# Performance work log

Hardware: AMD Instinct MI355X
Metric: run time of the kernel (lower is better)

Reference implementation:

```python
import jax, jax.numpy as jnp
import numpy as np
import math

BS, L, NNF, NEF = 8, 107, 17, 9
NH, EH, H3, NL, K = 128, 32, 32, 10, 3
PC, TL, TH, FF, NCLS = 32, 3, 8, 256, 3
D = NH + PC
HD = D // TH
RPG = 150
N = BS * L
E = BS * (2 * (L - 1) + RPG)
EPS = 1e-5


def _ln(z, g, b):
    m = z.mean(-1, keepdims=True)
    v = ((z - m) ** 2).mean(-1, keepdims=True)
    return (z - m) / jnp.sqrt(v + EPS) * g + b


def _gelu(z):
    return jax.nn.gelu(z, approximate=False)


def _forward(x, edge_attr, cheb_w, cheb_b, ee_w, ee_b, mlp_w1, mlp_b1, mlp_w2, mlp_b2,
             root_w, conv_b, ln_g, ln_b, attn_in_w, attn_in_b, attn_out_w, attn_out_b,
             ff_w1, ff_b1, ff_w2, ff_b2, tln1_g, tln1_b, tln2_g, tln2_b, lin_w, lin_b,
             seq_edge_index, edge_index):
    n = x.shape[0]
    # --- ChebConv (K=3, sym norm, lambda_max=2 -> L_hat = -D^-1/2 A D^-1/2) on seq edges ---
    ss, sd = seq_edge_index[0], seq_edge_index[1]
    deg = jax.ops.segment_sum(jnp.ones_like(ss, dtype=x.dtype), ss, num_segments=n)
    dinv = jnp.where(deg > 0, jax.lax.rsqrt(jnp.maximum(deg, 1e-12)), 0.0)
    w = -(dinv[ss] * dinv[sd])
    lap = lambda h: jax.ops.segment_sum(w[:, None] * h[ss], sd, num_segments=n)
    tx1 = lap(x)
    tx2 = 2.0 * lap(tx1) - x
    h = x @ cheb_w[0] + tx1 @ cheb_w[1] + tx2 @ cheb_w[2] + cheb_b

    # --- edge encoder ---
    ea = edge_attr @ ee_w + ee_b
    src, dst = edge_index[0], edge_index[1]

    # --- NNConv: per-edge weight W_e = MLP(ea) in R^{NHxNH}; gather-matmul-scatter ---
    def nnconv(h, l):
        we = ((ea @ mlp_w1[l] + mlp_b1[l]) @ mlp_w2[l] + mlp_b2[l]).reshape(-1, NH, NH)
        msg = jnp.einsum('ei,eio->eo', h[src], we)
        return jax.ops.segment_sum(msg, dst, num_segments=n) + h @ root_w[l] + conv_b[l]

    h = nnconv(h, 0)  # layers[0].conv applied directly (no residual)
    for l in range(1, NL):  # DeepGCNLayer res+: x + conv(gelu(LN(x)))
        h = h + nnconv(_gelu(_ln(h, ln_g[l], ln_b[l])), l)
    h = _gelu(_ln(h, ln_g[0], ln_b[0]))  # reuses layer 0's norm/act

    # --- sinusoidal position encoding (dim=PC), concat ---
    p = jnp.arange(L, dtype=x.dtype)[:, None]
    div = jnp.exp(jnp.arange(0, PC, 2, dtype=x.dtype) * (-math.log(10000.0) / PC))
    pos = jnp.zeros((L, PC), dtype=x.dtype)
    pos = pos.at[:, 0::2].set(jnp.sin(p * div)).at[:, 1::2].set(jnp.cos(p * div))

    t = jnp.concatenate([h.reshape(BS, L, NH), jnp.broadcast_to(pos, (BS, L, PC))], -1)

    # --- post-norm TransformerEncoder (relu FFN), vectorized over graphs ---
    scale = 1.0 / math.sqrt(HD)
    for l in range(TL):
        qkv = t @ attn_in_w[l] + attn_in_b[l]
        q, k, v = jnp.split(qkv, 3, axis=-1)
        q = q.reshape(BS, L, TH, HD)
        k = k.reshape(BS, L, TH, HD)
        v = v.reshape(BS, L, TH, HD)
        a = jax.nn.softmax(jnp.einsum('bqhd,bkhd->bhqk', q, k) * scale, axis=-1)
        o = jnp.einsum('bhqk,bkhd->bqhd', a, v).reshape(BS, L, D) @ attn_out_w[l] + attn_out_b[l]
        t = _ln(t + o, tln1_g[l], tln1_b[l])
        f = jax.nn.relu(t @ ff_w1[l] + ff_b1[l]) @ ff_w2[l] + ff_b2[l]
        t = _ln(t + f, tln2_g[l], tln2_b[l])

    return t.reshape(n, D) @ lin_w + lin_b


def setup_inputs():
    rng = np.random.default_rng(0)
    ks = iter(jax.random.split(jax.random.key(0), 40))
    # bidirectional sequence edges per graph + random pair edges
    base = np.arange(L - 1)
    s = np.concatenate([base, base + 1])
    d = np.concatenate([base + 1, base])
    off = (np.arange(BS) * L)[:, None]
    seq_src = (s[None] + off).ravel()
    seq_dst = (d[None] + off).ravel()
    r_src = (rng.integers(0, L, (BS, RPG)) + off).ravel()
    r_dst = (rng.integers(0, L, (BS, RPG)) + off).ravel()
    edge_index = jnp.asarray(np.stack([np.concatenate([seq_src, r_src]),
                                       np.concatenate([seq_dst, r_dst])]), dtype=jnp.int32)
    seq_edge_index = jnp.asarray(np.stack([seq_src, seq_dst]), dtype=jnp.int32)
    n_seq = seq_src.shape[0]

    def nrm(shape, sc=0.05):
        return jax.random.normal(next(ks), shape, dtype=jnp.float32) * sc

    x = jax.random.normal(next(ks), (N, NNF), dtype=jnp.float32)
    edge_attr = jax.random.normal(next(ks), (E, NEF), dtype=jnp.float32)
    col0 = jnp.concatenate([jnp.zeros((n_seq,), jnp.float32), jnp.ones((E - n_seq,), jnp.float32)])
    edge_attr = edge_attr.at[:, 0].set(col0)
    return {
        'x': x, 'edge_attr': edge_attr,
        'cheb_w': nrm((K, NNF, NH), 0.1), 'cheb_b': nrm((NH,), 0.02),
        'ee_w': nrm((NEF, EH), 0.1), 'ee_b': nrm((EH,), 0.02),
        'mlp_w1': nrm((NL, EH, H3), 0.1), 'mlp_b1': nrm((NL, H3), 0.02),
        'mlp_w2': nrm((NL, H3, NH * NH), 0.01), 'mlp_b2': nrm((NL, NH * NH), 0.01),
        'root_w': nrm((NL, NH, NH), 0.05), 'conv_b': nrm((NL, NH), 0.02),
        'ln_g': jnp.ones((NL, NH), jnp.float32), 'ln_b': jnp.zeros((NL, NH), jnp.float32),
        'attn_in_w': nrm((TL, D, 3 * D), 0.05), 'attn_in_b': nrm((TL, 3 * D), 0.02),
        'attn_out_w': nrm((TL, D, D), 0.05), 'attn_out_b': nrm((TL, D), 0.02),
        'ff_w1': nrm((TL, D, FF), 0.05), 'ff_b1': nrm((TL, FF), 0.02),
        'ff_w2': nrm((TL, FF, D), 0.05), 'ff_b2': nrm((TL, D), 0.02),
        'tln1_g': jnp.ones((TL, D), jnp.float32), 'tln1_b': jnp.zeros((TL, D), jnp.float32),
        'tln2_g': jnp.ones((TL, D), jnp.float32), 'tln2_b': jnp.zeros((TL, D), jnp.float32),
        'lin_w': nrm((D, NCLS), 0.05), 'lin_b': nrm((NCLS,), 0.02),
        'seq_edge_index': seq_edge_index, 'edge_index': edge_index,
    }


def reference(x, edge_attr, cheb_w, cheb_b, ee_w, ee_b, mlp_w1, mlp_b1, mlp_w2, mlp_b2,
              root_w, conv_b, ln_g, ln_b, attn_in_w, attn_in_b, attn_out_w, attn_out_b,
              ff_w1, ff_b1, ff_w2, ff_b2, tln1_g, tln1_b, tln2_g, tln2_b, lin_w, lin_b,
              seq_edge_index, edge_index):
    return _forward(x, edge_attr, cheb_w, cheb_b, ee_w, ee_b, mlp_w1, mlp_b1, mlp_w2, mlp_b2,
                    root_w, conv_b, ln_g, ln_b, attn_in_w, attn_in_b, attn_out_w, attn_out_b,
                    ff_w1, ff_b1, ff_w2, ff_b2, tln1_g, tln1_b, tln2_g, tln2_b, lin_w, lin_b,
                    seq_edge_index, edge_index)
```

## Files before the change

kernel.cpp:

```cpp
#include <hip/hip_runtime.h>
#include <hip/hip_bf16.h>
#include <math.h>

#define BSZ   8
#define LSEQ  107
#define NNF   17
#define NEF   9
#define NH    128
#define EHD   32
#define H3D   32
#define NLAY  10
#define PCD   32
#define TLAY  3
#define THD   8
#define FFD   256
#define NCLS  3
#define DD    160
#define HDD   20
#define NND   856
#define NPAD  896
#define NE    2896
#define CSTR  32
#define QKVP  512
#define PRJP  192
#define KTOT  1408
#define ALD2  1416

#define SB_CHEB 428
#define SB_PAD  (SB_CHEB)
#define SB_CSR1 (SB_PAD + 1)
#define SB_TPK  (SB_CSR1 + 1)
#define NTPK    171
#define SB_BIAS (SB_TPK + NTPK)
#define SB_E10  (SB_BIAS + 1)
#define NE10    114
#define SB_WT   (SB_E10 + NE10)
#define NWT     160
#define SB_TOT  (SB_WT + NWT)

typedef __bf16 bf16;
typedef __bf16 bf16x8 __attribute__((ext_vector_type(8)));
typedef float  f32x4  __attribute__((ext_vector_type(4)));

__device__ __forceinline__ float geluf(float z) {
    return 0.5f * z * (1.0f + erff(z * 0.70710678118654752f));
}
__device__ __forceinline__ float wred(float v) {
    #pragma unroll
    for (int o = 32; o; o >>= 1) v += __shfl_xor(v, o, 64);
    return v;
}
__device__ __forceinline__ float dinv_path(int n) {
    return (n == 0 || n == LSEQ - 1) ? 1.0f : 0.70710678118654752f;
}

__global__ __launch_bounds__(256) void k_setup(
        const float* __restrict__ x, const float* __restrict__ cw,
        const float* __restrict__ cb, bf16* __restrict__ zA, bf16* __restrict__ zB,
        const float* __restrict__ eattr, const float* __restrict__ eew,
        const float* __restrict__ eeb, const float* __restrict__ w1,
        const float* __restrict__ b1,
        const float* __restrict__ w2, const float* __restrict__ b2,
        const float* __restrict__ rootw, bf16* __restrict__ bpk,
        float* __restrict__ e10,
        const int* __restrict__ ei, int* __restrict__ deg, int* __restrict__ csr,
        const float* __restrict__ ain_w, const float* __restrict__ aow,
        const float* __restrict__ ffw1, const float* __restrict__ ffw2,
        const float* __restrict__ ain_b, const float* __restrict__ aob,
        const float* __restrict__ ffb1, const float* __restrict__ ffb2,
        bf16* __restrict__ bqkv, bf16* __restrict__ bproj,
        bf16* __restrict__ bff1, bf16* __restrict__ bff2,
        float* __restrict__ tb_bias) {
    __shared__ __align__(16) char sm[24576];
    int blk = blockIdx.x, tid = threadIdx.x;
    if (blk < SB_CHEB) {
        float (*xs)[5][NNF] = (float (*)[5][NNF])sm;
        int s = tid >> 7, o = tid & 127;
        int n = blk * 2 + s;
        int g = n / LSEQ, i = n - g * LSEQ;
        if (o < 5 * NNF) {
            int k = o / NNF, f = o - k * NNF;
            int p = i - 2 + k; p = p < 0 ? 0 : (p > LSEQ - 1 ? LSEQ - 1 : p);
            xs[s][k][f] = x[(g * LSEQ + p) * NNF + f];
        }
        __syncthreads();
        float di  = dinv_path(i);
        float dm1 = dinv_path(i - 1 < 0 ? 0 : i - 1);
        float dp1 = dinv_path(i + 1 > LSEQ - 1 ? LSEQ - 1 : i + 1);
        float dm2 = dinv_path(i - 2 < 0 ? 0 : i - 2);
        float dp2 = dinv_path(i + 2 > LSEQ - 1 ? LSEQ - 1 : i + 2);
        float wmc = (i > 0)        ? -(dm1 * di) : 0.f;
        float wpc = (i < LSEQ - 1) ? -(dp1 * di) : 0.f;
        float wmm = (i - 1 > 0)        ? -(dm2 * dm1) : 0.f;
        float wpm = -(di * dm1);
        float wmp = -(di * dp1);
        float wpp = (i + 1 < LSEQ - 1) ? -(dp2 * dp1) : 0.f;
        float acc = cb[o];
        #pragma unroll
        for (int f = 0; f < NNF; ++f) {
            float xm2 = xs[s][0][f], xm1 = xs[s][1][f], x0 = xs[s][2][f],
                  xp1 = xs[s][3][f], xp2 = xs[s][4][f];
            float t1c = wmc * xm1 + wpc * xp1;
            float t1m = wmm * xm2 + wpm * x0;
            float t1p = wmp * x0 + wpp * xp2;
            float t2 = 2.f * (wmc * t1m + wpc * t1p) - x0;
            acc += x0 * cw[f * NH + o] + t1c * cw[(NNF + f) * NH + o]
                 + t2 * cw[(2 * NNF + f) * NH + o];
        }
        zA[n * NH + o] = (bf16)acc;
    } else if (blk == SB_PAD) {
        for (int i = tid; i < (NPAD - NND) * NH; i += 256) {
            zA[NND * NH + i] = (bf16)0.f;
            zB[NND * NH + i] = (bf16)0.f;
        }
    } else if (blk == SB_CSR1) {
        int* ldeg = (int*)sm;
        for (int i = tid; i < NND; i += 256) ldeg[i] = 0;
        __syncthreads();
        for (int e = tid; e < NE; e += 256) {
            int d = ei[NE + e];
            int slot = atomicAdd(&ldeg[d], 1);
            if (slot < CSTR) csr[d * CSTR + slot] = e;
        }
        __syncthreads();
        for (int i = tid; i < NND; i += 256) deg[i] = ldeg[i];
    } else if (blk < SB_BIAS) {
        bf16 (*tt)[65] = (bf16 (*)[65])sm;
        int v = blk - SB_TPK;
        int tl = v / 57, t = v % 57;
        const float* src; bf16* dst; int Kd, srcN, ct, kt;
        if (t < 24)      { ct = t & 7;  kt = t >> 3;          src = ain_w + (size_t)tl * DD * 3 * DD; srcN = 3 * DD; Kd = DD;  dst = bqkv  + (size_t)tl * QKVP * DD; }
        else if (t < 33) { int u = t - 24; ct = u % 3; kt = u / 3; src = aow + (size_t)tl * DD * DD;  srcN = DD;     Kd = DD;  dst = bproj + (size_t)tl * PRJP * DD; }
        else if (t < 45) { int u = t - 33; ct = u % 4; kt = u / 4; src = ffw1 + (size_t)tl * DD * FFD; srcN = FFD;   Kd = DD;  dst = bff1  + (size_t)tl * FFD * DD; }
        else             { int u = t - 45; ct = u % 3; kt = u / 3; src = ffw2 + (size_t)tl * FFD * DD; srcN = DD;    Kd = FFD; dst = bff2  + (size_t)tl * PRJP * FFD; }
        int cc = tid & 63, rr = tid >> 6;
        #pragma unroll
        for (int rep = 0; rep < 16; ++rep) {
            int kl = rep * 4 + rr;
            int k = kt * 64 + kl;
            int col = ct * 64 + cc;
            float val = (k < Kd && col < srcN) ? src[(size_t)k * srcN + col] : 0.f;
            tt[kl][cc] = (bf16)val;
        }
        __syncthreads();
        int k = kt * 64 + cc;
        if (k < Kd) {
            #pragma unroll
            for (int rep = 0; rep < 16; ++rep) {
                int c = rep * 4 + rr;
                dst[(size_t)(ct * 64 + c) * Kd + k] = tt[cc][c];
            }
        }
    } else if (blk == SB_BIAS) {
        for (int i = tid; i < 3 * 1152; i += 256) {
            int tl = i / 1152, r = i % 1152;
            float val;
            if (r < 512)      { val = (r < 480) ? ain_b[tl * 480 + r] : 0.f; }
            else if (r < 704) { int c = r - 512; val = (c < 160) ? aob[tl * 160 + c] : 0.f; }
            else if (r < 960) { int c = r - 704; val = ffb1[tl * 256 + c]; }
            else              { int c = r - 960; val = (c < 160) ? ffb2[tl * 160 + c] : 0.f; }
            tb_bias[i] = val;
        }
    } else if (blk < SB_WT) {
        int idx = (blk - SB_E10) * 256 + tid;
        if (idx < NE * 10) {
            int e = idx / 10, f = idx - e * 10;
            e10[idx] = (f < NEF) ? eattr[e * NEF + f] : 1.0f;
        }
    } else {
        float* gw  = (float*)sm;
        bf16* ldsT = (bf16*)(sm + 2048);
        int v = blk - SB_WT;
        int l = v >> 4, chunk = v & 15;
        int io0 = chunk * 1024;
        for (int e = tid; e < 320; e += 256) {
            int f = e >> 5, j = e & 31;
            float acc;
            if (f < 9) {
                acc = 0.f;
                for (int m = 0; m < EHD; ++m)
                    acc += eew[f * EHD + m] * w1[(size_t)l * EHD * H3D + m * H3D + j];
            } else {
                acc = b1[l * H3D + j];
                for (int m = 0; m < EHD; ++m)
                    acc += eeb[m] * w1[(size_t)l * EHD * H3D + m * H3D + j];
            }
            gw[e] = acc;
        }
        __syncthreads();
        int io = io0 + tid * 4;
        const float* w2l = w2 + (size_t)l * 524288;
        float acc[10][4];
        float4 b2v = *(const float4*)(b2 + (size_t)l * 16384 + io);
        #pragma unroll
        for (int f = 0; f < 9; ++f) { acc[f][0] = 0.f; acc[f][1] = 0.f; acc[f][2] = 0.f; acc[f][3] = 0.f; }
        acc[9][0] = b2v.x; acc[9][1] = b2v.y; acc[9][2] = b2v.z; acc[9][3] = b2v.w;
        for (int j = 0; j < H3D; ++j) {
            float4 wv4 = *(const float4*)(w2l + (size_t)j * 16384 + io);
            #pragma unroll
            for (int f = 0; f < 10; ++f) {
                float gf = gw[f * 32 + j];
                acc[f][0] += gf * wv4.x; acc[f][1] += gf * wv4.y;
                acc[f][2] += gf * wv4.z; acc[f][3] += gf * wv4.w;
            }
        }
        int o4 = (tid & 31) * 4, il = tid >> 5;
        #pragma unroll
        for (int f = 0; f < 10; ++f)
            #pragma unroll
            for (int k = 0; k < 4; ++k)
                ldsT[(f * 128 + o4 + k) * 8 + il] = (bf16)acc[f][k];
        float4 rv = *(const float4*)(rootw + (size_t)l * 16384 + io);
        ldsT[(10 * 128 + o4 + 0) * 8 + il] = (bf16)rv.x;
        ldsT[(10 * 128 + o4 + 1) * 8 + il] = (bf16)rv.y;
        ldsT[(10 * 128 + o4 + 2) * 8 + il] = (bf16)rv.z;
        ldsT[(10 * 128 + o4 + 3) * 8 + il] = (bf16)rv.w;
        __syncthreads();
        if (tid < 128) {
            int o = tid;
            bf16* dst = bpk + (size_t)l * 128 * KTOT + (size_t)o * KTOT + chunk * 8;
            #pragma unroll
            for (int f = 0; f < 11; ++f) {
                bf16x8 val = *(bf16x8*)(ldsT + ((size_t)f * 128 + o) * 8);
                *(bf16x8*)(dst + f * 128) = val;
            }
        }
    }
}

__global__ __launch_bounds__(256) void k_layer(const bf16* __restrict__ zin,
                                               float* __restrict__ h,
                                               const float* __restrict__ e10,
                                               const bf16* __restrict__ bpkL,
                                               const float* __restrict__ conv_b,
                                               const float* __restrict__ lng,
                                               const float* __restrict__ lnb,
                                               bf16* __restrict__ zout,
                                               float* __restrict__ tbuf,
                                               const int* __restrict__ ei,
                                               const int* __restrict__ deg,
                                               const int* __restrict__ csr,
                                               int l) {
    __shared__ bf16 As[16][ALD2];
    __shared__ float outs[16][128];
    int tid = threadIdx.x, lane = tid & 63, wv = tid >> 6;
    int r0 = blockIdx.x * 16;
    for (int rr = 0; rr < 4; ++rr) {
        int r = wv * 4 + rr;
        int d = r0 + r;
        float acc[10][2];
        #pragma unroll
        for (int f = 0; f < 10; ++f) { acc[f][0] = 0.f; acc[f][1] = 0.f; }
        int dg = 0;
        if (d < NND) { dg = deg[d]; if (dg > CSTR) dg = CSTR; }
        for (int k = 0; k < dg; ++k) {
            int e = csr[d * CSTR + k];
            int s = ei[e];
            float z0 = (float)zin[s * NH + lane];
            float z1 = (float)zin[s * NH + lane + 64];
            const float* ew = e10 + e * 10;
            #pragma unroll
            for (int f = 0; f < 10; ++f) {
                float wf = ew[f];
                acc[f][0] += wf * z0;
                acc[f][1] += wf * z1;
            }
        }
        #pragma unroll
        for (int f = 0; f < 10; ++f) {
            As[r][f * 128 + lane] = (bf16)acc[f][0];
            As[r][f * 128 + lane + 64] = (bf16)acc[f][1];
        }
        As[r][1280 + lane] = zin[d * NH + lane];
        As[r][1280 + lane + 64] = zin[d * NH + lane + 64];
    }
    __syncthreads();
    {
        int rA = lane & 15, q = lane >> 4, q8 = q * 8;
        const bf16* Af = &As[rA][0];
        int cb0 = wv * 32;
        const bf16* B0 = bpkL + (size_t)(cb0 + rA) * KTOT;
        const bf16* B1 = bpkL + (size_t)(cb0 + 16 + rA) * KTOT;
        f32x4 ac0 = {0.f, 0.f, 0.f, 0.f}, ac1 = ac0;
        for (int ks = 0; ks < KTOT / 32; ++ks) {
            int kb = ks * 32 + q8;
            bf16x8 av = *(const bf16x8*)(Af + kb);
            bf16x8 b0 = *(const bf16x8*)(B0 + kb);
            bf16x8 b1 = *(const bf16x8*)(B1 + kb);
            ac0 = __builtin_amdgcn_mfma_f32_16x16x32_bf16(av, b0, ac0, 0, 0, 0);
            ac1 = __builtin_amdgcn_mfma_f32_16x16x32_bf16(av, b1, ac1, 0, 0, 0);
        }
        #pragma unroll
        for (int reg = 0; reg < 4; ++reg) {
            outs[q * 4 + reg][cb0 + rA] = ac0[reg];
            outs[q * 4 + reg][cb0 + 16 + rA] = ac1[reg];
        }
    }
    __syncthreads();
    for (int rr = 0; rr < 4; ++rr) {
        int r = wv * 4 + rr;
        int d = r0 + r;
        if (d >= NND) {
            if (l < NLAY - 1) {
                zout[d * NH + lane] = (bf16)0.f;
                zout[d * NH + lane + 64] = (bf16)0.f;
            }
            continue;
        }
        float v0 = outs[r][lane] + conv_b[l * NH + lane];
        float v1 = outs[r][lane + 64] + conv_b[l * NH + lane + 64];
        if (l > 0) {
            v0 += h[d * NH + lane];
            v1 += h[d * NH + lane + 64];
        }
        if (l < NLAY - 1) {
            h[d * NH + lane] = v0;
            h[d * NH + lane + 64] = v1;
        }
        float m = wred(v0 + v1) * (1.f / NH);
        float d0 = v0 - m, d1 = v1 - m;
        float var = wred(d0 * d0 + d1 * d1) * (1.f / NH);
        float rs = rsqrtf(var + 1e-5f);
        if (l < NLAY - 1) {
            int ln = l + 1;
            zout[d * NH + lane] = (bf16)geluf(d0 * rs * lng[ln * NH + lane] + lnb[ln * NH + lane]);
            zout[d * NH + lane + 64] = (bf16)geluf(d1 * rs * lng[ln * NH + lane + 64] + lnb[ln * NH + lane + 64]);
        } else {
            tbuf[(size_t)d * DD + lane] = geluf(d0 * rs * lng[lane] + lnb[lane]);
            tbuf[(size_t)d * DD + lane + 64] = geluf(d1 * rs * lng[lane + 64] + lnb[lane + 64]);
        }
    }
    if (l == NLAY - 1) {
        for (int idx = tid; idx < 16 * PCD; idx += 256) {
            int r = idx >> 5, pc = idx & 31;
            int d = r0 + r;
            if (d < NND) {
                int qq = d % LSEQ;
                float twoi = (float)(pc & ~1);
                float ang = (float)qq * expf(-twoi * 0.28782313662425572f);
                tbuf[(size_t)d * DD + NH + pc] = (pc & 1) ? cosf(ang) : sinf(ang);
            }
        }
    }
}

__global__ __launch_bounds__(256) void k_gmm(const float* __restrict__ A,
                                             const bf16* __restrict__ bp,
                                             const float* __restrict__ biasP,
                                             float* __restrict__ C,
                                             int ksteps, int K, int PW, int act) {
    int lane = threadIdx.x & 63, wv = threadIdx.x >> 6;
    int m0 = blockIdx.y * 64 + wv * 16;
    int ct = blockIdx.x;
    int r = lane & 15, q = lane >> 4, q8 = q * 8;
    const float* Arow = A + (size_t)(m0 + r) * K;
    const bf16* Bb = bp + ((size_t)ct * 64 + r) * K;
    f32x4 a0 = {0.f,0.f,0.f,0.f}, a1 = a0, a2 = a0, a3 = a0;
    for (int ks = 0; ks < ksteps; ++ks) {
        int kb = ks * 32 + q8;
        float4 f0 = *(const float4*)(Arow + kb);
        float4 f1 = *(const float4*)(Arow + kb + 4);
        bf16x8 av;
        av[0] = (bf16)f0.x; av[1] = (bf16)f0.y; av[2] = (bf16)f0.z; av[3] = (bf16)f0.w;
        av[4] = (bf16)f1.x; av[5] = (bf16)f1.y; av[6] = (bf16)f1.z; av[7] = (bf16)f1.w;
        bf16x8 b0 = *(const bf16x8*)(Bb + 0 * 16 * K + kb);
        bf16x8 b1 = *(const bf16x8*)(Bb + 1 * 16 * K + kb);
        bf16x8 b2 = *(const bf16x8*)(Bb + 2 * 16 * K + kb);
        bf16x8 b3 = *(const bf16x8*)(Bb + 3 * 16 * K + kb);
        a0 = __builtin_amdgcn_mfma_f32_16x16x32_bf16(av, b0, a0, 0, 0, 0);
        a1 = __builtin_amdgcn_mfma_f32_16x16x32_bf16(av, b1, a1, 0, 0, 0);
        a2 = __builtin_amdgcn_mfma_f32_16x16x32_bf16(av, b2, a2, 0, 0, 0);
        a3 = __builtin_amdgcn_mfma_f32_16x16x32_bf16(av, b3, a3, 0, 0, 0);
    }
    int cb = ct * 64;
    #pragma unroll
    for (int reg = 0; reg < 4; ++reg) {
        float* Crow = C + (size_t)(m0 + q * 4 + reg) * PW + cb;
        float v0 = a0[reg] + biasP[cb + 0 * 16 + r];
        float v1 = a1[reg] + biasP[cb + 1 * 16 + r];
        float v2 = a2[reg] + biasP[cb + 2 * 16 + r];
        float v3 = a3[reg] + biasP[cb + 3 * 16 + r];
        if (act) { v0 = fmaxf(v0, 0.f); v1 = fmaxf(v1, 0.f); v2 = fmaxf(v2, 0.f); v3 = fmaxf(v3, 0.f); }
        Crow[0 * 16 + r] = v0;
        Crow[1 * 16 + r] = v1;
        Crow[2 * 16 + r] = v2;
        Crow[3 * 16 + r] = v3;
    }
}

__global__ __launch_bounds__(256) void k_pln(const float* __restrict__ A,
                                             const bf16* __restrict__ bp,
                                             const float* __restrict__ biasP,
                                             int ksteps, int K,
                                             float* __restrict__ t,
                                             const float* __restrict__ g,
                                             const float* __restrict__ bvec,
                                             int tail,
                                             const bf16* __restrict__ tbp,
                                             const float* __restrict__ tbias_,
                                             float* __restrict__ tout,
                                             const float* __restrict__ lw,
                                             const float* __restrict__ lb,
                                             float* __restrict__ outp) {
    __shared__ float outs[16][PRJP];
    __shared__ bf16 Als[16][176];
    int tid = threadIdx.x, lane = tid & 63, wv = tid >> 6;
    int m0 = blockIdx.x * 16;
    if (wv < 3) {
        int r = lane & 15, q = lane >> 4, q8 = q * 8;
        const float* Arow = A + (size_t)(m0 + r) * K;
        const bf16* Bb = bp + ((size_t)wv * 64 + r) * K;
        f32x4 a0 = {0.f,0.f,0.f,0.f}, a1 = a0, a2 = a0, a3 = a0;
        for (int ks = 0; ks < ksteps; ++ks) {
            int kb = ks * 32 + q8;
            float4 f0 = *(const float4*)(Arow + kb);
            float4 f1 = *(const float4*)(Arow + kb + 4);
            bf16x8 av;
            av[0] = (bf16)f0.x; av[1] = (bf16)f0.y; av[2] = (bf16)f0.z; av[3] = (bf16)f0.w;
            av[4] = (bf16)f1.x; av[5] = (bf16)f1.y; av[6] = (bf16)f1.z; av[7] = (bf16)f1.w;
            bf16x8 b0 = *(const bf16x8*)(Bb + 0 * 16 * K + kb);
            bf16x8 b1 = *(const bf16x8*)(Bb + 1 * 16 * K + kb);
            bf16x8 b2 = *(const bf16x8*)(Bb + 2 * 16 * K + kb);
            bf16x8 b3 = *(const bf16x8*)(Bb + 3 * 16 * K + kb);
            a0 = __builtin_amdgcn_mfma_f32_16x16x32_bf16(av, b0, a0, 0, 0, 0);
            a1 = __builtin_amdgcn_mfma_f32_16x16x32_bf16(av, b1, a1, 0, 0, 0);
            a2 = __builtin_amdgcn_mfma_f32_16x16x32_bf16(av, b2, a2, 0, 0, 0);
            a3 = __builtin_amdgcn_mfma_f32_16x16x32_bf16(av, b3, a3, 0, 0, 0);
        }
        int cb = wv * 64;
        #pragma unroll
        for (int reg = 0; reg < 4; ++reg) {
            int rw = q * 4 + reg;
            outs[rw][cb + 0 * 16 + r] = a0[reg] + biasP[cb + 0 * 16 + r];
            outs[rw][cb + 1 * 16 + r] = a1[reg] + biasP[cb + 1 * 16 + r];
            outs[rw][cb + 2 * 16 + r] = a2[reg] + biasP[cb + 2 * 16 + r];
            outs[rw][cb + 3 * 16 + r] = a3[reg] + biasP[cb + 3 * 16 + r];
        }
    }
    __syncthreads();
    for (int rr = 0; rr < 4; ++rr) {
        int r = wv * 4 + rr;
        int d = m0 + r;
        if (d >= NND) continue;
        int c0 = lane, c1 = lane + 64, c2 = lane + 128;
        float v0 = outs[r][c0] + t[(size_t)d * DD + c0];
        float v1 = outs[r][c1] + t[(size_t)d * DD + c1];
        float v2 = (lane < 32) ? (outs[r][c2] + t[(size_t)d * DD + c2]) : 0.f;
        float m = wred(v0 + v1 + v2) * (1.f / DD);
        float d0 = v0 - m, d1 = v1 - m, d2 = (lane < 32) ? (v2 - m) : 0.f;
        float var = wred(d0 * d0 + d1 * d1 + d2 * d2) * (1.f / DD);
        float rs = rsqrtf(var + 1e-5f);
        float n0 = d0 * rs * g[c0] + bvec[c0];
        float n1 = d1 * rs * g[c1] + bvec[c1];
        float n2 = (lane < 32) ? (d2 * rs * g[c2] + bvec[c2]) : 0.f;
        t[(size_t)d * DD + c0] = n0;
        t[(size_t)d * DD + c1] = n1;
        if (lane < 32) t[(size_t)d * DD + c2] = n2;
        Als[r][c0] = (bf16)n0;
        Als[r][c1] = (bf16)n1;
        if (lane < 32) Als[r][c2] = (bf16)n2;
        if (tail == 0 && outp) {
            #pragma unroll
            for (int cls = 0; cls < NCLS; ++cls) {
                float part = n0 * lw[c0 * NCLS + cls] + n1 * lw[c1 * NCLS + cls]
                           + ((lane < 32) ? n2 * lw[c2 * NCLS + cls] : 0.f);
                float tot = wred(part);
                if (lane == 0) outp[d * NCLS + cls] = tot + lb[cls];
            }
        }
    }
    if (!tail) return;
    __syncthreads();
    {
        int PW = (tail == 1) ? FFD : QKVP;
        int ntile = (tail == 1) ? 1 : 2;
        int rA = lane & 15, q = lane >> 4, q8 = q * 8;
        for (int ctl = 0; ctl < ntile; ++ctl) {
            int cb = (ctl * 4 + wv) * 64;
            const bf16* Bb = tbp + ((size_t)cb + rA) * DD;
            f32x4 a0 = {0.f,0.f,0.f,0.f}, a1 = a0, a2 = a0, a3 = a0;
            #pragma unroll
            for (int ks = 0; ks < 5; ++ks) {
                int kb = ks * 32 + q8;
                bf16x8 av = *(const bf16x8*)(&Als[rA][0] + kb);
                bf16x8 b0 = *(const bf16x8*)(Bb + 0 * 16 * DD + kb);
                bf16x8 b1 = *(const bf16x8*)(Bb + 1 * 16 * DD + kb);
                bf16x8 b2 = *(const bf16x8*)(Bb + 2 * 16 * DD + kb);
                bf16x8 b3 = *(const bf16x8*)(Bb + 3 * 16 * DD + kb);
                a0 = __builtin_amdgcn_mfma_f32_16x16x32_bf16(av, b0, a0, 0, 0, 0);
                a1 = __builtin_amdgcn_mfma_f32_16x16x32_bf16(av, b1, a1, 0, 0, 0);
                a2 = __builtin_amdgcn_mfma_f32_16x16x32_bf16(av, b2, a2, 0, 0, 0);
                a3 = __builtin_amdgcn_mfma_f32_16x16x32_bf16(av, b3, a3, 0, 0, 0);
            }
            #pragma unroll
            for (int reg = 0; reg < 4; ++reg) {
                float* Crow = tout + (size_t)(m0 + q * 4 + reg) * PW + cb;
                float v0 = a0[reg] + tbias_[cb + 0 * 16 + rA];
                float v1 = a1[reg] + tbias_[cb + 1 * 16 + rA];
                float v2 = a2[reg] + tbias_[cb + 2 * 16 + rA];
                float v3 = a3[reg] + tbias_[cb + 3 * 16 + rA];
                if (tail == 1) { v0 = fmaxf(v0, 0.f); v1 = fmaxf(v1, 0.f); v2 = fmaxf(v2, 0.f); v3 = fmaxf(v3, 0.f); }
                Crow[0 * 16 + rA] = v0;
                Crow[1 * 16 + rA] = v1;
                Crow[2 * 16 + rA] = v2;
                Crow[3 * 16 + rA] = v3;
            }
        }
    }
}

#define UPD4(ac, V) { ac.x = ac.x * corr + p * V.x; ac.y = ac.y * corr + p * V.y; \
                      ac.z = ac.z * corr + p * V.z; ac.w = ac.w * corr + p * V.w; }
__global__ __launch_bounds__(64) void k_attn(const float* __restrict__ qkv,
                                             float* __restrict__ aout) {
    __shared__ float4 Ks4[LSEQ * 5], Vs4[LSEQ * 5];
    int bh = blockIdx.x;
    int b = bh >> 3, hh = bh & 7;
    int tid = threadIdx.x;
    for (int i = tid; i < LSEQ * 5; i += 64) {
        int kq = i / 5, c4 = i - kq * 5;
        const float* rowp = qkv + (size_t)(b * LSEQ + kq) * QKVP + hh * HDD;
        Ks4[i] = ((const float4*)(rowp + DD))[c4];
        Vs4[i] = ((const float4*)(rowp + 2 * DD))[c4];
    }
    __syncthreads();
    int q = blockIdx.y * 64 + tid;
    if (q >= LSEQ) return;
    const float4* qp = (const float4*)(qkv + (size_t)(b * LSEQ + q) * QKVP + hh * HDD);
    float4 q0 = qp[0], q1 = qp[1], q2 = qp[2], q3 = qp[3], q4 = qp[4];
    const float scale = 0.22360679774997896f;
    float mx = -3.0e38f, sum = 0.f;
    float4 z = {0.f, 0.f, 0.f, 0.f};
    float4 ac0 = z, ac1 = z, ac2 = z, ac3 = z, ac4 = z;
    for (int k = 0; k < LSEQ; ++k) {
        const float4* kp = Ks4 + k * 5;
        float4 K0 = kp[0], K1 = kp[1], K2 = kp[2], K3 = kp[3], K4 = kp[4];
        float a0 = q0.x * K0.x + q0.y * K0.y + q0.z * K0.z + q0.w * K0.w;
        float a1 = q1.x * K1.x + q1.y * K1.y + q1.z * K1.z + q1.w * K1.w;
        float a2 = q2.x * K2.x + q2.y * K2.y + q2.z * K2.z + q2.w * K2.w;
        float a3 = q3.x * K3.x + q3.y * K3.y + q3.z * K3.z + q3.w * K3.w;
        float a4 = q4.x * K4.x + q4.y * K4.y + q4.z * K4.z + q4.w * K4.w;
        float s = (((a0 + a1) + (a2 + a3)) + a4) * scale;
        float mn = fmaxf(mx, s);
        float corr = __expf(mx - mn);
        float p = __expf(s - mn);
        mx = mn;
        sum = sum * corr + p;
        const float4* vp = Vs4 + k * 5;
        float4 V0 = vp[0], V1 = vp[1], V2 = vp[2], V3 = vp[3], V4 = vp[4];
        UPD4(ac0, V0); UPD4(ac1, V1); UPD4(ac2, V2); UPD4(ac3, V3); UPD4(ac4, V4);
    }
    float inv = 1.f / sum;
    float4* op = (float4*)(aout + (size_t)(b * LSEQ + q) * DD + hh * HDD);
    float4 o0 = {ac0.x * inv, ac0.y * inv, ac0.z * inv, ac0.w * inv};
    float4 o1 = {ac1.x * inv, ac1.y * inv, ac1.z * inv, ac1.w * inv};
    float4 o2 = {ac2.x * inv, ac2.y * inv, ac2.z * inv, ac2.w * inv};
    float4 o3 = {ac3.x * inv, ac3.y * inv, ac3.z * inv, ac3.w * inv};
    float4 o4 = {ac4.x * inv, ac4.y * inv, ac4.z * inv, ac4.w * inv};
    op[0] = o0; op[1] = o1; op[2] = o2; op[3] = o3; op[4] = o4;
}

extern "C" void kernel_launch(void* const* d_in, const int* in_sizes, int n_in,
                              void* d_out, int out_size, void* d_ws, size_t ws_size,
                              hipStream_t stream) {
    (void)in_sizes; (void)n_in; (void)out_size; (void)ws_size;
    const float* x      = (const float*)d_in[0];
    const float* eattr  = (const float*)d_in[1];
    const float* cheb_w = (const float*)d_in[2];
    const float* cheb_b = (const float*)d_in[3];
    const float* ee_w   = (const float*)d_in[4];
    const float* ee_b   = (const float*)d_in[5];
    const float* mlp_w1 = (const float*)d_in[6];
    const float* mlp_b1 = (const float*)d_in[7];
    const float* mlp_w2 = (const float*)d_in[8];
    const float* mlp_b2 = (const float*)d_in[9];
    const float* root_w = (const float*)d_in[10];
    const float* conv_b = (const float*)d_in[11];
    const float* ln_g   = (const float*)d_in[12];
    const float* ln_b   = (const float*)d_in[13];
    const float* ain_w  = (const float*)d_in[14];
    const float* ain_b  = (const float*)d_in[15];
    const float* aow    = (const float*)d_in[16];
    const float* aob    = (const float*)d_in[17];
    const float* ffw1   = (const float*)d_in[18];
    const float* ffb1   = (const float*)d_in[19];
    const float* ffw2   = (const float*)d_in[20];
    const float* ffb2   = (const float*)d_in[21];
    const float* t1g    = (const float*)d_in[22];
    const float* t1b    = (const float*)d_in[23];
    const float* t2g    = (const float*)d_in[24];
    const float* t2b    = (const float*)d_in[25];
    const float* lin_w  = (const float*)d_in[26];
    const float* lin_b  = (const float*)d_in[27];
    const int* ei       = (const int*)d_in[29];

    char* w = (char*)d_ws;
    size_t off = 0;
    auto alloc = [&](size_t bytes) -> void* {
        void* p = w + off;
        off += (bytes + 255) & ~(size_t)255;
        return p;
    };
    bf16*  bpk   = (bf16*)alloc((size_t)NLAY * 128 * KTOT * 2);
    float* e10   = (float*)alloc((size_t)NE * 10 * 4);
    float* h     = (float*)alloc((size_t)NND * NH * 4);
    bf16*  zA    = (bf16*)alloc((size_t)NPAD * NH * 2);
    bf16*  zB    = (bf16*)alloc((size_t)NPAD * NH * 2);
    float* tbuf  = (float*)alloc((size_t)NPAD * DD * 4);
    float* qkvC  = (float*)alloc((size_t)NPAD * QKVP * 4);
    float* abuf  = (float*)alloc((size_t)NPAD * DD * 4);
    float* f1    = (float*)alloc((size_t)NPAD * FFD * 4);
    int*   deg   = (int*)alloc((size_t)NND * 4);
    int*   csr   = (int*)alloc((size_t)NND * CSTR * 4);
    bf16*  bqkv  = (bf16*)alloc((size_t)TLAY * QKVP * DD * 2);
    bf16*  bproj = (bf16*)alloc((size_t)TLAY * PRJP * DD * 2);
    bf16*  bff1  = (bf16*)alloc((size_t)TLAY * FFD * DD * 2);
    bf16*  bff2  = (bf16*)alloc((size_t)TLAY * PRJP * FFD * 2);
    float* tbias = (float*)alloc((size_t)TLAY * 1152 * 4);

    k_setup<<<SB_TOT, 256, 0, stream>>>(x, cheb_w, cheb_b, zA, zB,
                                        eattr, ee_w, ee_b, mlp_w1, mlp_b1,
                                        mlp_w2, mlp_b2, root_w, bpk, e10,
                                        ei, deg, csr,
                                        ain_w, aow, ffw1, ffw2,
                                        ain_b, aob, ffb1, ffb2,
                                        bqkv, bproj, bff1, bff2, tbias);

    bf16* zcur = zA;
    bf16* znxt = zB;
    for (int l = 0; l < NLAY; ++l) {
        k_layer<<<NPAD / 16, 256, 0, stream>>>(zcur, h, e10, bpk + (size_t)l * 128 * KTOT,
                                               conv_b, ln_g, ln_b, znxt, tbuf,
                                               ei, deg, csr, l);
        bf16* tmp = zcur; zcur = znxt; znxt = tmp;
    }

    k_gmm<<<dim3(QKVP / 64, 14), 256, 0, stream>>>(tbuf, bqkv, tbias, qkvC, 5, DD, QKVP, 0);
    for (int tl = 0; tl < TLAY; ++tl) {
        const float* bb = tbias + (size_t)tl * 1152;
        k_attn<<<dim3(BSZ * THD, 2), 64, 0, stream>>>(qkvC, abuf);
        k_pln<<<NPAD / 16, 256, 0, stream>>>(abuf, bproj + (size_t)tl * PRJP * DD, bb + 512,
                                             5, DD, tbuf,
                                             t1g + (size_t)tl * DD, t1b + (size_t)tl * DD,
                                             1, bff1 + (size_t)tl * FFD * DD, bb + 704, f1,
                                             nullptr, nullptr, nullptr);
        int last = (tl == TLAY - 1);
        k_pln<<<NPAD / 16, 256, 0, stream>>>(f1, bff2 + (size_t)tl * PRJP * FFD, bb + 960,
                                             8, FFD, tbuf,
                                             t2g + (size_t)tl * DD, t2b + (size_t)tl * DD,
                                             last ? 0 : 2,
                                             last ? nullptr : bqkv + (size_t)(tl + 1) * QKVP * DD,
                                             last ? nullptr : tbias + (size_t)(tl + 1) * 1152,
                                             last ? nullptr : qkvC,
                                             last ? lin_w : nullptr,
                                             last ? lin_b : nullptr,
                                             last ? (float*)d_out : nullptr);
    }
}
```

Measured before the change: 538.8 us.

## Pre-gather edge sources and features into CSR; vectorize gathers; split MFMA accumulators

The setup kernel now writes each incoming edge's source index and its 9 edge features, plus a trailing 1.0, directly into per-destination CSR slots. This replaces the separate e10 buffer and the edge-id indirection that every layer kernel went through. The layer kernel's neighbour gather uses bf16x2 loads and stores, with each lane handling adjacent columns. The MFMA K-loop is split into two halves with independent accumulators to increase instruction-level parallelism. In exchange, the single CSR-building block does more serial writes, and the CSR feature buffer is larger than the old e10 buffer.

```diff
diff --git a/kernel.cpp b/kernel.cpp
--- a/kernel.cpp
+++ b/kernel.cpp
@@ -32,13 +32,12 @@
 #define SB_TPK  (SB_CSR1 + 1)
 #define NTPK    171
 #define SB_BIAS (SB_TPK + NTPK)
-#define SB_E10  (SB_BIAS + 1)
-#define NE10    114
-#define SB_WT   (SB_E10 + NE10)
+#define SB_WT   (SB_BIAS + 1)
 #define NWT     160
 #define SB_TOT  (SB_WT + NWT)
 
 typedef __bf16 bf16;
+typedef __bf16 bf16x2 __attribute__((ext_vector_type(2)));
 typedef __bf16 bf16x8 __attribute__((ext_vector_type(8)));
 typedef float  f32x4  __attribute__((ext_vector_type(4)));
 
@@ -62,8 +61,8 @@
         const float* __restrict__ b1,
         const float* __restrict__ w2, const float* __restrict__ b2,
         const float* __restrict__ rootw, bf16* __restrict__ bpk,
-        float* __restrict__ e10,
-        const int* __restrict__ ei, int* __restrict__ deg, int* __restrict__ csr,
+        const int* __restrict__ ei, int* __restrict__ deg,
+        int* __restrict__ csrs, float* __restrict__ csrw,
         const float* __restrict__ ain_w, const float* __restrict__ aow,
         const float* __restrict__ ffw1, const float* __restrict__ ffw2,
         const float* __restrict__ ain_b, const float* __restrict__ aob,
@@ -120,7 +119,14 @@
         for (int e = tid; e < NE; e += 256) {
             int d = ei[NE + e];
             int slot = atomicAdd(&ldeg[d], 1);
-            if (slot < CSTR) csr[d * CSTR + slot] = e;
+            if (slot < CSTR) {
+                int idx = d * CSTR + slot;
+                csrs[idx] = ei[e];
+                float* wp = csrw + (size_t)idx * 10;
+                #pragma unroll
+                for (int f = 0; f < NEF; ++f) wp[f] = eattr[e * NEF + f];
+                wp[9] = 1.0f;
+            }
         }
         __syncthreads();
         for (int i = tid; i < NND; i += 256) deg[i] = ldeg[i];
@@ -160,12 +166,6 @@
             else if (r < 960) { int c = r - 704; val = ffb1[tl * 256 + c]; }
             else              { int c = r - 960; val = (c < 160) ? ffb2[tl * 160 + c] : 0.f; }
             tb_bias[i] = val;
-        }
-    } else if (blk < SB_WT) {
-        int idx = (blk - SB_E10) * 256 + tid;
-        if (idx < NE * 10) {
-            int e = idx / 10, f = idx - e * 10;
-            e10[idx] = (f < NEF) ? eattr[e * NEF + f] : 1.0f;
         }
     } else {
         float* gw  = (float*)sm;
@@ -230,16 +230,15 @@
 
 __global__ __launch_bounds__(256) void k_layer(const bf16* __restrict__ zin,
                                                float* __restrict__ h,
-                                               const float* __restrict__ e10,
                                                const bf16* __restrict__ bpkL,
                                                const float* __restrict__ conv_b,
                                                const float* __restrict__ lng,
                                                const float* __restrict__ lnb,
                                                bf16* __restrict__ zout,
                                                float* __restrict__ tbuf,
-                                               const int* __restrict__ ei,
                                                const int* __restrict__ deg,
-                                               const int* __restrict__ csr,
+                                               const int* __restrict__ csrs,
+                                               const float* __restrict__ csrw,
                                                int l) {
     __shared__ bf16 As[16][ALD2];
     __shared__ float outs[16][128];
@@ -254,25 +253,25 @@
         int dg = 0;
         if (d < NND) { dg = deg[d]; if (dg > CSTR) dg = CSTR; }
         for (int k = 0; k < dg; ++k) {
-            int e = csr[d * CSTR + k];
-            int s = ei[e];
-            float z0 = (float)zin[s * NH + lane];
-            float z1 = (float)zin[s * NH + lane + 64];
-            const float* ew = e10 + e * 10;
+            int idx = d * CSTR + k;
+            int s = csrs[idx];
+            bf16x2 zz = *(const bf16x2*)(zin + (size_t)s * NH + 2 * lane);
+            float z0 = (float)zz[0], z1 = (float)zz[1];
+            const float* ww = csrw + (size_t)idx * 10;
             #pragma unroll
             for (int f = 0; f < 10; ++f) {
-                float wf = ew[f];
+                float wf = ww[f];
                 acc[f][0] += wf * z0;
                 acc[f][1] += wf * z1;
             }
         }
         #pragma unroll
         for (int f = 0; f < 10; ++f) {
-            As[r][f * 128 + lane] = (bf16)acc[f][0];
-            As[r][f * 128 + lane + 64] = (bf16)acc[f][1];
-        }
-        As[r][1280 + lane] = zin[d * NH + lane];
-        As[r][1280 + lane + 64] = zin[d * NH + lane + 64];
+            bf16x2 av; av[0] = (bf16)acc[f][0]; av[1] = (bf16)acc[f][1];
+            *(bf16x2*)(&As[r][f * 128 + 2 * lane]) = av;
+        }
+        bf16x2 zr = *(const bf16x2*)(zin + (size_t)d * NH + 2 * lane);
+        *(bf16x2*)(&As[r][1280 + 2 * lane]) = zr;
     }
     __syncthreads();
     {
@@ -281,19 +280,30 @@
         int cb0 = wv * 32;
         const bf16* B0 = bpkL + (size_t)(cb0 + rA) * KTOT;
         const bf16* B1 = bpkL + (size_t)(cb0 + 16 + rA) * KTOT;
-        f32x4 ac0 = {0.f, 0.f, 0.f, 0.f}, ac1 = ac0;
-        for (int ks = 0; ks < KTOT / 32; ++ks) {
+        f32x4 zf = {0.f, 0.f, 0.f, 0.f};
+        f32x4 a0a = zf, a1a = zf, a0b = zf, a1b = zf;
+        #pragma unroll 2
+        for (int ks = 0; ks < 22; ++ks) {
             int kb = ks * 32 + q8;
             bf16x8 av = *(const bf16x8*)(Af + kb);
             bf16x8 b0 = *(const bf16x8*)(B0 + kb);
             bf16x8 b1 = *(const bf16x8*)(B1 + kb);
-            ac0 = __builtin_amdgcn_mfma_f32_16x16x32_bf16(av, b0, ac0, 0, 0, 0);
-            ac1 = __builtin_amdgcn_mfma_f32_16x16x32_bf16(av, b1, ac1, 0, 0, 0);
+            a0a = __builtin_amdgcn_mfma_f32_16x16x32_bf16(av, b0, a0a, 0, 0, 0);
+            a1a = __builtin_amdgcn_mfma_f32_16x16x32_bf16(av, b1, a1a, 0, 0, 0);
+        }
+        #pragma unroll 2
+        for (int ks = 22; ks < 44; ++ks) {
+            int kb = ks * 32 + q8;
+            bf16x8 av = *(const bf16x8*)(Af + kb);
+            bf16x8 b0 = *(const bf16x8*)(B0 + kb);
+            bf16x8 b1 = *(const bf16x8*)(B1 + kb);
+            a0b = __builtin_amdgcn_mfma_f32_16x16x32_bf16(av, b0, a0b, 0, 0, 0);
+            a1b = __builtin_amdgcn_mfma_f32_16x16x32_bf16(av, b1, a1b, 0, 0, 0);
         }
         #pragma unroll
         for (int reg = 0; reg < 4; ++reg) {
-            outs[q * 4 + reg][cb0 + rA] = ac0[reg];
-            outs[q * 4 + reg][cb0 + 16 + rA] = ac1[reg];
+            outs[q * 4 + reg][cb0 + rA] = a0a[reg] + a0b[reg];
+            outs[q * 4 + reg][cb0 + 16 + rA] = a1a[reg] + a1b[reg];
         }
     }
     __syncthreads();
@@ -602,7 +612,6 @@
         return p;
     };
     bf16*  bpk   = (bf16*)alloc((size_t)NLAY * 128 * KTOT * 2);
-    float* e10   = (float*)alloc((size_t)NE * 10 * 4);
     float* h     = (float*)alloc((size_t)NND * NH * 4);
     bf16*  zA    = (bf16*)alloc((size_t)NPAD * NH * 2);
     bf16*  zB    = (bf16*)alloc((size_t)NPAD * NH * 2);
@@ -611,7 +620,8 @@
     float* abuf  = (float*)alloc((size_t)NPAD * DD * 4);
     float* f1    = (float*)alloc((size_t)NPAD * FFD * 4);
     int*   deg   = (int*)alloc((size_t)NND * 4);
-    int*   csr   = (int*)alloc((size_t)NND * CSTR * 4);
+    int*   csrs  = (int*)alloc((size_t)NND * CSTR * 4);
+    float* csrw  = (float*)alloc((size_t)NND * CSTR * 10 * 4);
     bf16*  bqkv  = (bf16*)alloc((size_t)TLAY * QKVP * DD * 2);
     bf16*  bproj = (bf16*)alloc((size_t)TLAY * PRJP * DD * 2);
     bf16*  bff1  = (bf16*)alloc((size_t)TLAY * FFD * DD * 2);
@@ -620,8 +630,8 @@
 
     k_setup<<<SB_TOT, 256, 0, stream>>>(x, cheb_w, cheb_b, zA, zB,
                                         eattr, ee_w, ee_b, mlp_w1, mlp_b1,
-                                        mlp_w2, mlp_b2, root_w, bpk, e10,
-                                        ei, deg, csr,
+                                        mlp_w2, mlp_b2, root_w, bpk,
+                                        ei, deg, csrs, csrw,
                                         ain_w, aow, ffw1, ffw2,
                                         ain_b, aob, ffb1, ffb2,
                                         bqkv, bproj, bff1, bff2, tbias);
@@ -629,9 +639,9 @@
     bf16* zcur = zA;
     bf16* znxt = zB;
     for (int l = 0; l < NLAY; ++l) {
-        k_layer<<<NPAD / 16, 256, 0, stream>>>(zcur, h, e10, bpk + (size_t)l * 128 * KTOT,
+        k_layer<<<NPAD / 16, 256, 0, stream>>>(zcur, h, bpk + (size_t)l * 128 * KTOT,
                                                conv_b, ln_g, ln_b, znxt, tbuf,
-                                               ei, deg, csr, l);
+                                               deg, csrs, csrw, l);
         bf16* tmp = zcur; zcur = znxt; znxt = tmp;
     }
 
```

Result: faster. 523.9 us (-2.8%).
